# Performance work log

Hardware: AMD Instinct MI355X
Metric: run time of the kernel (lower is better)

Reference implementation:

```python
import jax, jax.numpy as jnp
import numpy as np

B, S, HID = 1, 2048, 4096
H, HKV, D = 32, 8, 128
ROT = 64  # partial_rotary_factor = 0.5
EPS = 1e-6
SCALE = D ** -0.5


def setup_inputs() -> dict:
    key = jax.random.key(0)
    ks = jax.random.split(key, 8)
    return {
        "hidden_states": jax.random.normal(ks[0], (B, S, HID), jnp.float32),
        "cos": jax.random.uniform(ks[1], (B, S, ROT), jnp.float32),
        "sin": jax.random.uniform(ks[2], (B, S, ROT), jnp.float32),
        "Wq": jax.random.normal(ks[3], (H * D, HID), jnp.float32) * 0.02,
        "Wk": jax.random.normal(ks[4], (HKV * D, HID), jnp.float32) * 0.02,
        "Wv": jax.random.normal(ks[5], (HKV * D, HID), jnp.float32) * 0.02,
        "Wo": jax.random.normal(ks[6], (H * D, HID), jnp.float32).T * 0.02,  # [HID, H*D]
        "q_norm_w": jnp.ones((D,), jnp.float32),
        "k_norm_w": jnp.ones((D,), jnp.float32),
    }


def _rmsnorm(x, w):
    var = jnp.mean(jnp.square(x), axis=-1, keepdims=True)
    return x * jax.lax.rsqrt(var + EPS) * w


def _rotate_half(x):
    x1, x2 = jnp.split(x, 2, axis=-1)
    return jnp.concatenate([-x2, x1], axis=-1)


def reference(hidden_states, cos, sin, Wq, Wk, Wv, Wo, q_norm_w, k_norm_w):
    b, s, _ = hidden_states.shape
    q = (hidden_states @ Wq.T).reshape(b, s, H, D)
    k = (hidden_states @ Wk.T).reshape(b, s, HKV, D)
    v = (hidden_states @ Wv.T).reshape(b, s, HKV, D)
    # per-head QK RMSNorm
    q = _rmsnorm(q, q_norm_w)
    k = _rmsnorm(k, k_norm_w)
    # partial RoPE on first ROT dims; cos/sin broadcast over head dim (unsqueeze_dim=2)
    cs = cos[:, :, None, :]  # [B,S,1,ROT]
    sn = sin[:, :, None, :]
    q_rot, q_pass = q[..., :ROT], q[..., ROT:]
    k_rot, k_pass = k[..., :ROT], k[..., ROT:]
    q_rot = q_rot * cs + _rotate_half(q_rot) * sn
    k_rot = k_rot * cs + _rotate_half(k_rot) * sn
    q = jnp.concatenate([q_rot, q_pass], axis=-1)
    k = jnp.concatenate([k_rot, k_pass], axis=-1)
    # GQA: expand kv heads to query heads
    rep = H // HKV
    k = jnp.repeat(k, rep, axis=2)  # [B,S,H,D]
    v = jnp.repeat(v, rep, axis=2)
    # causal SDPA, bsnd layout
    scores = jnp.einsum("bqhd,bkhd->bhqk", q, k) * SCALE
    causal = jnp.tril(jnp.ones((s, s), bool))
    scores = jnp.where(causal, scores, jnp.finfo(scores.dtype).min)
    attn = jax.nn.softmax(scores, axis=-1)
    out = jnp.einsum("bhqk,bkhd->bqhd", attn, v).reshape(b, s, H * D)
    return out @ Wo.T
```

## Files before the change

### kernel.cpp

```cpp
#include <hip/hip_runtime.h>
#include <hip/hip_bf16.h>

typedef __attribute__((ext_vector_type(8))) short bf16x8;
typedef __attribute__((ext_vector_type(4))) float f32x4;
typedef __hip_bfloat16 bf16;

#define S_LEN 2048
#define HIDDEN 4096
#define NH 32
#define NKV 8
#define DH 128
#define ROTD 64
#define QKVW 6144
#define KOFF 4096
#define VOFF 5120
#define ATT_SCALE 0.08838834764831845f
#define RMS_EPS 1e-6f
#define KPITCH 136
#define VPITCH 72

#define BAR() __builtin_amdgcn_s_barrier()
#define VMCNT(n) asm volatile("s_waitcnt vmcnt(" #n ")" ::: "memory")
#define LGKM(n)  asm volatile("s_waitcnt lgkmcnt(" #n ")" ::: "memory")

static __device__ __forceinline__ unsigned short f2bu(float f) {
    bf16 h = __float2bfloat16(f);
    return __builtin_bit_cast(unsigned short, h);
}

static __device__ __forceinline__ void load_lds_16(const bf16* g, bf16* l) {
    __builtin_amdgcn_global_load_lds((const __attribute__((address_space(1))) void*)g,
                                     (__attribute__((address_space(3))) void*)l, 16, 0, 0);
}

__global__ __launch_bounds__(256) void cast_f32_bf16(const float* __restrict__ src,
                                                     unsigned short* __restrict__ dst, int n4) {
    int i = blockIdx.x * 256 + threadIdx.x;
    if (i >= n4) return;
    float4 v = reinterpret_cast<const float4*>(src)[i];
    ushort4 o;
    o.x = f2bu(v.x); o.y = f2bu(v.y); o.z = f2bu(v.z); o.w = f2bu(v.w);
    reinterpret_cast<ushort4*>(dst)[i] = o;
}

__global__ __launch_bounds__(256) void add_f32(float* __restrict__ dst,
                                               const float* __restrict__ src, int n4) {
    int i = blockIdx.x * 256 + threadIdx.x;
    if (i >= n4) return;
    float4 a = reinterpret_cast<float4*>(dst)[i];
    float4 b = reinterpret_cast<const float4*>(src)[i];
    a.x += b.x; a.y += b.y; a.z += b.z; a.w += b.w;
    reinterpret_cast<float4*>(dst)[i] = a;
}

#define LDA_SUB(bufi, half) do {                                                        \
    const bf16* _ab = &As[bufi][half][0];                                               \
    _Pragma("unroll") for (int mf = 0; mf < 4; ++mf) {                                  \
        const int _r = arow + mf * 16;                                                  \
        _Pragma("unroll") for (int kk = 0; kk < 2; ++kk)                                \
            av[mf][kk] = *reinterpret_cast<const bf16x8*>(                              \
                _ab + (((_r << 6) + kk * 32 + quad * 8) ^ xorv));                       \
    } } while (0)

#define LDB_SUB(bufi, half, set) do {                                                   \
    const bf16* _bb = &Bs[bufi][half][0];                                               \
    _Pragma("unroll") for (int nf = 0; nf < 2; ++nf) {                                  \
        const int _r = brow + nf * 16;                                                  \
        _Pragma("unroll") for (int kk = 0; kk < 2; ++kk)                                \
            bv[set][nf][kk] = *reinterpret_cast<const bf16x8*>(                         \
                _bb + (((_r << 6) + kk * 32 + quad * 8) ^ xorv));                       \
    } } while (0)

#define MMQ(mh, nh, set) do {                                                           \
    _Pragma("unroll") for (int mf = 0; mf < 4; ++mf)                                    \
    _Pragma("unroll") for (int nf = 0; nf < 2; ++nf)                                    \
    _Pragma("unroll") for (int kk = 0; kk < 2; ++kk)                                    \
        acc[mh][nh][mf][nf] = __builtin_amdgcn_mfma_f32_16x16x32_bf16(                  \
            av[mf][kk], bv[set][nf][kk], acc[mh][nh][mf][nf], 0, 0, 0);                 \
    } while (0)

#define STAGE_A(bufi, half, tau) do {                                                   \
    const bf16* _s = Abase + (size_t)(half) * 128 * K + (size_t)(tau) * 64;             \
    load_lds_16(_s + sro0, &As[bufi][half][e0]);                                        \
    load_lds_16(_s + sro1, &As[bufi][half][e1]); } while (0)

#define STAGE_B(bufi, half, tau) do {                                                   \
    const bf16* _s = Bbase + (size_t)(half) * 128 * K + (size_t)(tau) * 64;             \
    load_lds_16(_s + sro0, &Bs[bufi][half][e0]);                                        \
    load_lds_16(_s + sro1, &Bs[bufi][half][e1]); } while (0)

template <typename OutT>
__global__ __launch_bounds__(512, 2) void gemm256(const bf16* __restrict__ A,
                                                  const bf16* __restrict__ B,
                                                  OutT* __restrict__ C,
                                                  OutT* __restrict__ C2,
                                                  int M, int N, int K, int ktiles) {
    __shared__ bf16 As[2][2][128 * 64];
    __shared__ bf16 Bs[2][2][128 * 64];

    const int tid  = threadIdx.x;
    const int lane = tid & 63;
    const int lq   = lane & 15;
    const int quad = lane >> 4;
    const int wave = tid >> 6;
    const int wr   = wave >> 2;
    const int wc   = wave & 3;

    const int nwg = gridDim.x;
    const int cpx = nwg >> 3;
    const int wg  = (blockIdx.x & 7) * cpx + (blockIdx.x >> 3);
    const int ntn = N >> 8;
    const int m0  = (wg / ntn) << 8;
    const int n0  = (wg % ntn) << 8;
    const int ksl = blockIdx.y;

    const int NT = ktiles;

    const int d0 = tid * 16;
    const int d1 = 8192 + tid * 16;
    const int o0 = d0 ^ (((d0 >> 7) & 7) << 4);
    const int o1 = d1 ^ (((d1 >> 7) & 7) << 4);
    const int e0 = d0 >> 1;
    const int e1 = d1 >> 1;
    const size_t sro0 = (size_t)((o0 >> 1) >> 6) * K + ((o0 >> 1) & 63);
    const size_t sro1 = (size_t)((o1 >> 1) >> 6) * K + ((o1 >> 1) & 63);
    const bf16* Abase = A + (size_t)m0 * K + (size_t)ksl * ktiles * 64;
    const bf16* Bbase = B + (size_t)n0 * K + (size_t)ksl * ktiles * 64;
    OutT* __restrict__ Cw = ksl ? C2 : C;

    const int arow = wr * 64 + lq;
    const int brow = wc * 32 + lq;
    const int xorv = (lq & 7) << 3;

    f32x4  acc[2][2][4][2] = {};
    bf16x8 av[4][2];
    bf16x8 bv[2][2][2];

    STAGE_B(0, 0, 0); STAGE_A(0, 0, 0); STAGE_B(0, 1, 0); STAGE_A(0, 1, 0);
    STAGE_B(1, 0, 1); STAGE_A(1, 0, 1); STAGE_B(1, 1, 1);
    VMCNT(6);
    BAR();

    for (int t = 0; t < NT; ++t) {
        const int buf = t & 1;

        LDA_SUB(buf, 0);
        LDB_SUB(buf, 0, 0);
        if (t + 1 < NT) STAGE_A(buf ^ 1, 1, t + 1);
        LGKM(8);
        BAR();
        LGKM(0);
        __builtin_amdgcn_s_setprio(1);
        MMQ(0, 0, 0);
        __builtin_amdgcn_s_setprio(0);
        BAR();

        LDB_SUB(buf, 1, 1);
        if (t + 2 < NT) STAGE_B(buf, 0, t + 2);
        BAR();
        LGKM(0);
        __builtin_amdgcn_s_setprio(1);
        MMQ(0, 1, 1);
        __builtin_amdgcn_s_setprio(0);
        BAR();

        LDA_SUB(buf, 1);
        if (t + 2 < NT) STAGE_A(buf, 0, t + 2);
        BAR();
        LGKM(0);
        __builtin_amdgcn_s_setprio(1);
        MMQ(1, 1, 1);
        __builtin_amdgcn_s_setprio(0);
        BAR();

        if (t + 2 < NT) STAGE_B(buf, 1, t + 2);
        BAR();
        __builtin_amdgcn_s_setprio(1);
        MMQ(1, 0, 0);
        __builtin_amdgcn_s_setprio(0);
        if (t < NT - 2) { VMCNT(6); } else { VMCNT(0); }
        BAR();
    }

#pragma unroll
    for (int mh = 0; mh < 2; ++mh)
#pragma unroll
        for (int nh = 0; nh < 2; ++nh)
#pragma unroll
            for (int mf = 0; mf < 4; ++mf)
#pragma unroll
                for (int nf = 0; nf < 2; ++nf)
#pragma unroll
                    for (int r = 0; r < 4; ++r) {
                        const int row = m0 + mh * 128 + wr * 64 + mf * 16 + quad * 4 + r;
                        const int col = n0 + nh * 128 + wc * 32 + nf * 16 + lq;
                        const float v = acc[mh][nh][mf][nf][r];
                        const size_t idx = (size_t)row * N + col;
                        if constexpr (sizeof(OutT) == 2) Cw[idx] = __float2bfloat16(v);
                        else                             Cw[idx] = v;
                    }
}

__global__ __launch_bounds__(256) void norm_rope(bf16* __restrict__ buf,
                                                 const float* __restrict__ w,
                                                 const float* __restrict__ cosp,
                                                 const float* __restrict__ sinp,
                                                 int log2nh, int stride, int coloff) {
    const int lane = threadIdx.x & 63;
    const int wave = threadIdx.x >> 6;
    const int row  = blockIdx.x * 4 + wave;
    const int s    = row >> log2nh;
    const int hh   = row & ((1 << log2nh) - 1);
    bf16* p = buf + (size_t)s * stride + coloff + hh * DH;

    float x1 = __bfloat162float(p[lane]);
    float x2 = __bfloat162float(p[64 + lane]);

    float ss = x1 * x1 + x2 * x2;
#pragma unroll
    for (int off = 1; off < 64; off <<= 1) ss += __shfl_xor(ss, off);
    float rs = rsqrtf(ss * (1.0f / 128.0f) + RMS_EPS);

    float y1 = x1 * rs * w[lane];
    float y2 = x2 * rs * w[64 + lane];

    float partner = __shfl_xor(y1, 32);
    float c  = cosp[(size_t)s * ROTD + lane];
    float sn = sinp[(size_t)s * ROTD + lane];
    float rot = (lane < 32) ? (y1 * c - partner * sn) : (y1 * c + partner * sn);

    p[lane]      = __float2bfloat16(rot);
    p[64 + lane] = __float2bfloat16(y2);
}

__global__ __launch_bounds__(256) void transpose_v(const bf16* __restrict__ v,
                                                   bf16* __restrict__ vt,
                                                   int stride, int colofs) {
    __shared__ bf16 t[32][65];
    const int c0 = blockIdx.x * 32;
    const int s0 = blockIdx.y * 64;
    {
        const int j  = threadIdx.x & 31;
        const int i0 = threadIdx.x >> 5;
#pragma unroll
        for (int p = 0; p < 8; ++p) {
            int si = p * 8 + i0;
            t[j][si] = v[(size_t)(s0 + si) * stride + colofs + c0 + j];
        }
    }
    __syncthreads();
    {
        const int ii = threadIdx.x & 63;
        const int j0 = threadIdx.x >> 6;
#pragma unroll
        for (int p = 0; p < 8; ++p) {
            int c = p * 4 + j0;
            vt[(size_t)(c0 + c) * S_LEN + s0 + ii] = t[c][ii];
        }
    }
}

struct FlashSmem {
    bf16 Ks[64][KPITCH];
    bf16 Vs[128][VPITCH];
    bf16 Ps[4][16][VPITCH];
};

static __device__ __forceinline__ void attn_qblock(int q0, int n_iter, int h, int kvh,
                                                   const bf16* __restrict__ QKV,
                                                   const bf16* __restrict__ VT,
                                                   bf16* __restrict__ O,
                                                   FlashSmem* sm) {
    const int tid  = threadIdx.x;
    const int lane = tid & 63;
    const int wave = tid >> 6;
    const int lq   = lane & 15;
    const int quad = lane >> 4;
    const int qr0  = q0 + wave * 16;

    bf16x8 qf[4];
    const bf16* qrow = QKV + (size_t)(qr0 + lq) * QKVW + h * DH + quad * 8;
#pragma unroll
    for (int i = 0; i < 4; ++i) {
        bf16x8 qv = *reinterpret_cast<const bf16x8*>(qrow + 32 * i);
#pragma unroll
        for (int j = 0; j < 8; ++j) {
            bf16 b = __builtin_bit_cast(bf16, (unsigned short)qv[j]);
            qv[j] = (short)__builtin_bit_cast(unsigned short,
                        __float2bfloat16(__bfloat162float(b) * ATT_SCALE));
        }
        qf[i] = qv;
    }

    f32x4 o[8];
#pragma unroll
    for (int t2 = 0; t2 < 8; ++t2) o[t2] = (f32x4){0.f, 0.f, 0.f, 0.f};
    float m_i[4], l_i[4];
#pragma unroll
    for (int r = 0; r < 4; ++r) { m_i[r] = -1e30f; l_i[r] = 0.f; }

    const bf16* kg = QKV + (size_t)(tid >> 2) * QKVW + KOFF + kvh * DH + (tid & 3) * 32;
    const bf16* vg = VT + (size_t)(kvh * DH + (tid >> 1)) * S_LEN + (tid & 1) * 32;
    bf16* ksl = &sm->Ks[tid >> 2][(tid & 3) * 32];
    bf16* vsl = &sm->Vs[tid >> 1][(tid & 1) * 32];
    bf16* pb  = &sm->Ps[wave][0][0];

    bf16x8 kreg[4], vreg[4];
#pragma unroll
    for (int c = 0; c < 4; ++c) {
        kreg[c] = *reinterpret_cast<const bf16x8*>(kg + 8 * c);
        vreg[c] = *reinterpret_cast<const bf16x8*>(vg + 8 * c);
    }

    for (int kt = 0; kt < n_iter; ++kt) {
        const int k0 = kt * 64;
#pragma unroll
        for (int c = 0; c < 4; ++c) {
            *reinterpret_cast<bf16x8*>(ksl + 8 * c) = kreg[c];
            *reinterpret_cast<bf16x8*>(vsl + 8 * c) = vreg[c];
        }
        __syncthreads();
        if (kt + 1 < n_iter) {
            const size_t kadv = (size_t)(kt + 1) * 64;
#pragma unroll
            for (int c = 0; c < 4; ++c) {
                kreg[c] = *reinterpret_cast<const bf16x8*>(kg + kadv * QKVW + 8 * c);
                vreg[c] = *reinterpret_cast<const bf16x8*>(vg + kadv + 8 * c);
            }
        }

        float p[4][4];
#pragma unroll
        for (int t = 0; t < 4; ++t) {
            f32x4 sacc = (f32x4){0.f, 0.f, 0.f, 0.f};
#pragma unroll
            for (int i = 0; i < 4; ++i) {
                bf16x8 kf = *reinterpret_cast<const bf16x8*>(&sm->Ks[t * 16 + lq][quad * 8 + 32 * i]);
                sacc = __builtin_amdgcn_mfma_f32_16x16x32_bf16(qf[i], kf, sacc, 0, 0, 0);
            }
#pragma unroll
            for (int r = 0; r < 4; ++r) {
                int qi = qr0 + quad * 4 + r;
                int ki = k0 + t * 16 + lq;
                p[t][r] = (ki > qi) ? -1e30f : sacc[r];
            }
        }

        float rowmax[4];
#pragma unroll
        for (int r = 0; r < 4; ++r)
            rowmax[r] = fmaxf(fmaxf(p[0][r], p[1][r]), fmaxf(p[2][r], p[3][r]));
#pragma unroll
        for (int off = 1; off < 16; off <<= 1)
#pragma unroll
            for (int r = 0; r < 4; ++r) rowmax[r] = fmaxf(rowmax[r], __shfl_xor(rowmax[r], off));

        float alpha[4];
#pragma unroll
        for (int r = 0; r < 4; ++r) {
            float mn = fmaxf(m_i[r], rowmax[r]);
            alpha[r] = __expf(m_i[r] - mn);
            m_i[r] = mn;
        }
#pragma unroll
        for (int t = 0; t < 4; ++t)
#pragma unroll
            for (int r = 0; r < 4; ++r) p[t][r] = __expf(p[t][r] - m_i[r]);

        float rsum[4];
#pragma unroll
        for (int r = 0; r < 4; ++r) rsum[r] = (p[0][r] + p[1][r]) + (p[2][r] + p[3][r]);
#pragma unroll
        for (int off = 1; off < 16; off <<= 1)
#pragma unroll
            for (int r = 0; r < 4; ++r) rsum[r] += __shfl_xor(rsum[r], off);
#pragma unroll
        for (int r = 0; r < 4; ++r) l_i[r] = l_i[r] * alpha[r] + rsum[r];

#pragma unroll
        for (int t = 0; t < 4; ++t)
#pragma unroll
            for (int r = 0; r < 4; ++r)
                pb[(quad * 4 + r) * VPITCH + t * 16 + lq] = __float2bfloat16(p[t][r]);
        __threadfence_block();

#pragma unroll
        for (int t2 = 0; t2 < 8; ++t2)
#pragma unroll
            for (int r = 0; r < 4; ++r) o[t2][r] *= alpha[r];

#pragma unroll
        for (int hh = 0; hh < 2; ++hh) {
            bf16x8 pa = *reinterpret_cast<const bf16x8*>(pb + lq * VPITCH + hh * 32 + quad * 8);
#pragma unroll
            for (int t2 = 0; t2 < 8; ++t2) {
                bf16x8 vf = *reinterpret_cast<const bf16x8*>(&sm->Vs[t2 * 16 + lq][hh * 32 + quad * 8]);
                o[t2] = __builtin_amdgcn_mfma_f32_16x16x32_bf16(pa, vf, o[t2], 0, 0, 0);
            }
        }
        __syncthreads();
    }

#pragma unroll
    for (int r = 0; r < 4; ++r) l_i[r] = 1.0f / l_i[r];
#pragma unroll
    for (int t2 = 0; t2 < 8; ++t2)
#pragma unroll
        for (int r = 0; r < 4; ++r)
            O[(size_t)(qr0 + quad * 4 + r) * (NH * DH) + h * DH + t2 * 16 + lq] =
                __float2bfloat16(o[t2][r] * l_i[r]);
}

__global__ __launch_bounds__(256) void flash_attn(const bf16* __restrict__ QKV,
                                                  const bf16* __restrict__ VT,
                                                  bf16* __restrict__ O) {
    __shared__ FlashSmem sm;
    const int b  = blockIdx.x;
    const int h  = b & 31;
    const int pr = b >> 5;
    const int kvh = h >> 2;
    attn_qblock((31 - pr) * 64, 32 - pr, h, kvh, QKV, VT, O, &sm);
    __syncthreads();
    attn_qblock(pr * 64,        pr + 1,  h, kvh, QKV, VT, O, &sm);
}

extern "C" void kernel_launch(void* const* d_in, const int* in_sizes, int n_in,
                              void* d_out, int out_size, void* d_ws, size_t ws_size,
                              hipStream_t stream) {
    const float* hs   = (const float*)d_in[0];
    const float* cosp = (const float*)d_in[1];
    const float* sinp = (const float*)d_in[2];
    const float* Wq   = (const float*)d_in[3];
    const float* Wk   = (const float*)d_in[4];
    const float* Wv   = (const float*)d_in[5];
    const float* Wo   = (const float*)d_in[6];
    const float* qw   = (const float*)d_in[7];
    const float* kw   = (const float*)d_in[8];
    float* out = (float*)d_out;

    char* ws = (char*)d_ws;
    size_t off = 0;
    auto carve = [&](size_t bytes) { char* p = ws + off; off += (bytes + 255) & ~(size_t)255; return p; };

    bf16* hsb  = (bf16*)carve((size_t)S_LEN * HIDDEN * 2);
    bf16* wqkv = (bf16*)carve((size_t)QKVW * HIDDEN * 2);
    bf16* wob  = (bf16*)carve((size_t)HIDDEN * NH * DH * 2);
    bf16* qkv  = (bf16*)carve((size_t)S_LEN * QKVW * 2);
    bf16* vtb  = (bf16*)carve((size_t)NKV * DH * S_LEN * 2);

    cast_f32_bf16<<<(S_LEN * HIDDEN / 4 + 255) / 256, 256, 0, stream>>>(hs, (unsigned short*)hsb, S_LEN * HIDDEN / 4);
    cast_f32_bf16<<<(NH * DH * HIDDEN / 4 + 255) / 256, 256, 0, stream>>>(Wq, (unsigned short*)wqkv, NH * DH * HIDDEN / 4);
    cast_f32_bf16<<<(NKV * DH * HIDDEN / 4 + 255) / 256, 256, 0, stream>>>(Wk, (unsigned short*)(wqkv + (size_t)KOFF * HIDDEN), NKV * DH * HIDDEN / 4);
    cast_f32_bf16<<<(NKV * DH * HIDDEN / 4 + 255) / 256, 256, 0, stream>>>(Wv, (unsigned short*)(wqkv + (size_t)VOFF * HIDDEN), NKV * DH * HIDDEN / 4);
    cast_f32_bf16<<<(HIDDEN * NH * DH / 4 + 255) / 256, 256, 0, stream>>>(Wo, (unsigned short*)wob, HIDDEN * NH * DH / 4);

    gemm256<bf16><<<dim3((S_LEN / 256) * (QKVW / 256), 1), 512, 0, stream>>>(
        hsb, wqkv, qkv, qkv, S_LEN, QKVW, HIDDEN, HIDDEN / 64);

    norm_rope<<<S_LEN * NH / 4, 256, 0, stream>>>(qkv, qw, cosp, sinp, 5, QKVW, 0);
    norm_rope<<<S_LEN * NKV / 4, 256, 0, stream>>>(qkv, kw, cosp, sinp, 3, QKVW, KOFF);

    transpose_v<<<dim3(NKV * DH / 32, S_LEN / 64), 256, 0, stream>>>(qkv, vtb, QKVW, VOFF);

    bf16* aob = hsb;
    flash_attn<<<512, 256, 0, stream>>>(qkv, vtb, aob);

    float* p1 = (float*)wqkv;
    gemm256<float><<<dim3((S_LEN / 256) * (HIDDEN / 256), 2), 512, 0, stream>>>(
        aob, wob, out, p1, S_LEN, HIDDEN, NH * DH, (NH * DH) / 2 / 64);

    add_f32<<<(S_LEN * HIDDEN / 4 + 255) / 256, 256, 0, stream>>>(out, p1, S_LEN * HIDDEN / 4);
}
```

Baseline: 539.7 us.

## Split attention KV range across two wave groups with LDS-direct swizzled K loads

The flash attention kernel now runs 512 threads per block, split into two groups of four waves that each process alternate 64-key tiles for the same query rows. Their partial softmax states are merged through LDS at the end. K tiles are loaded straight into LDS with XOR-swizzled global_load_lds, and V fragments are read directly from the transposed global buffer instead of being staged in LDS. This aims to raise parallelism and cut LDS staging cost. In exchange it adds a final merge step, exposes global-load latency on the V path, and idles one group on the last round when the tile count is odd.

New measurement: 607.7 us. 12.6% more time.

```diff
diff --git a/kernel.cpp b/kernel.cpp
--- a/kernel.cpp
+++ b/kernel.cpp
@@ -16,7 +16,6 @@
 #define VOFF 5120
 #define ATT_SCALE 0.08838834764831845f
 #define RMS_EPS 1e-6f
-#define KPITCH 136
 #define VPITCH 72
 
 #define BAR() __builtin_amdgcn_s_barrier()
@@ -261,9 +260,8 @@
 }
 
 struct FlashSmem {
-    bf16 Ks[64][KPITCH];
-    bf16 Vs[128][VPITCH];
-    bf16 Ps[4][16][VPITCH];
+    bf16 Ks[2][64][128];
+    bf16 Ps[8][16][VPITCH];
 };
 
 static __device__ __forceinline__ void attn_qblock(int q0, int n_iter, int h, int kvh,
@@ -274,9 +272,11 @@
     const int tid  = threadIdx.x;
     const int lane = tid & 63;
     const int wave = tid >> 6;
+    const int wq   = wave & 3;
+    const int g    = wave >> 2;
     const int lq   = lane & 15;
     const int quad = lane >> 4;
-    const int qr0  = q0 + wave * 16;
+    const int qr0  = q0 + wq * 16;
 
     bf16x8 qf[4];
     const bf16* qrow = QKV + (size_t)(qr0 + lq) * QKVW + h * DH + quad * 8;
@@ -285,9 +285,9 @@
         bf16x8 qv = *reinterpret_cast<const bf16x8*>(qrow + 32 * i);
 #pragma unroll
         for (int j = 0; j < 8; ++j) {
-            bf16 b = __builtin_bit_cast(bf16, (unsigned short)qv[j]);
+            bf16 bb = __builtin_bit_cast(bf16, (unsigned short)qv[j]);
             qv[j] = (short)__builtin_bit_cast(unsigned short,
-                        __float2bfloat16(__bfloat162float(b) * ATT_SCALE));
+                        __float2bfloat16(__bfloat162float(bb) * ATT_SCALE));
         }
         qf[i] = qv;
     }
@@ -299,121 +299,155 @@
 #pragma unroll
     for (int r = 0; r < 4; ++r) { m_i[r] = -1e30f; l_i[r] = 0.f; }
 
-    const bf16* kg = QKV + (size_t)(tid >> 2) * QKVW + KOFF + kvh * DH + (tid & 3) * 32;
-    const bf16* vg = VT + (size_t)(kvh * DH + (tid >> 1)) * S_LEN + (tid & 1) * 32;
-    bf16* ksl = &sm->Ks[tid >> 2][(tid & 3) * 32];
-    bf16* vsl = &sm->Vs[tid >> 1][(tid & 1) * 32];
+    const int d0 = tid * 16;
+    const int d1 = 8192 + tid * 16;
+    const int r0 = d0 >> 8;
+    const int r1 = d1 >> 8;
+    const int c0 = ((d0 ^ ((r0 & 7) << 4)) & 255) >> 1;
+    const int c1 = ((d1 ^ ((r1 & 7) << 4)) & 255) >> 1;
+    const bf16* Kg = QKV + (size_t)KOFF + kvh * DH;
+    const size_t so0 = (size_t)r0 * QKVW + c0;
+    const size_t so1 = (size_t)r1 * QKVW + c1;
+    bf16* ksb = &sm->Ks[0][0][0];
     bf16* pb  = &sm->Ps[wave][0][0];
-
-    bf16x8 kreg[4], vreg[4];
-#pragma unroll
-    for (int c = 0; c < 4; ++c) {
-        kreg[c] = *reinterpret_cast<const bf16x8*>(kg + 8 * c);
-        vreg[c] = *reinterpret_cast<const bf16x8*>(vg + 8 * c);
-    }
-
-    for (int kt = 0; kt < n_iter; ++kt) {
-        const int k0 = kt * 64;
-#pragma unroll
-        for (int c = 0; c < 4; ++c) {
-            *reinterpret_cast<bf16x8*>(ksl + 8 * c) = kreg[c];
-            *reinterpret_cast<bf16x8*>(vsl + 8 * c) = vreg[c];
-        }
-        __syncthreads();
-        if (kt + 1 < n_iter) {
-            const size_t kadv = (size_t)(kt + 1) * 64;
-#pragma unroll
-            for (int c = 0; c < 4; ++c) {
-                kreg[c] = *reinterpret_cast<const bf16x8*>(kg + kadv * QKVW + 8 * c);
-                vreg[c] = *reinterpret_cast<const bf16x8*>(vg + kadv + 8 * c);
+    const bf16* vb = VT + (size_t)(kvh * DH + lq) * S_LEN + quad * 8;
+
+    const int nrounds = (n_iter + 1) >> 1;
+    for (int rr = 0; rr < nrounds; ++rr) {
+        const int kt0 = 2 * rr;
+        {
+            const bf16* s0 = Kg + (size_t)kt0 * 64 * QKVW;
+            load_lds_16(s0 + so0, ksb + (d0 >> 1));
+            load_lds_16(s0 + so1, ksb + (d1 >> 1));
+            if (kt0 + 1 < n_iter) {
+                const bf16* s1 = s0 + (size_t)64 * QKVW;
+                load_lds_16(s1 + so0, ksb + 8192 + (d0 >> 1));
+                load_lds_16(s1 + so1, ksb + 8192 + (d1 >> 1));
             }
         }
-
-        float p[4][4];
-#pragma unroll
-        for (int t = 0; t < 4; ++t) {
-            f32x4 sacc = (f32x4){0.f, 0.f, 0.f, 0.f};
-#pragma unroll
-            for (int i = 0; i < 4; ++i) {
-                bf16x8 kf = *reinterpret_cast<const bf16x8*>(&sm->Ks[t * 16 + lq][quad * 8 + 32 * i]);
-                sacc = __builtin_amdgcn_mfma_f32_16x16x32_bf16(qf[i], kf, sacc, 0, 0, 0);
+        VMCNT(0);
+        BAR();
+
+        const int ktg = kt0 + g;
+        if (ktg < n_iter) {
+            const int k0 = ktg * 64;
+            const char* ksg = (const char*)(ksb + g * 8192);
+
+            float p[4][4];
+#pragma unroll
+            for (int t = 0; t < 4; ++t) {
+                f32x4 sacc = (f32x4){0.f, 0.f, 0.f, 0.f};
+#pragma unroll
+                for (int i = 0; i < 4; ++i) {
+                    const int krow = t * 16 + lq;
+                    const int kb = (krow << 8) + ((quad * 8 + 32 * i) << 1);
+                    bf16x8 kf = *reinterpret_cast<const bf16x8*>(ksg + (kb ^ ((krow & 7) << 4)));
+                    sacc = __builtin_amdgcn_mfma_f32_16x16x32_bf16(qf[i], kf, sacc, 0, 0, 0);
+                }
+#pragma unroll
+                for (int r = 0; r < 4; ++r) {
+                    int qi = qr0 + quad * 4 + r;
+                    int ki = k0 + t * 16 + lq;
+                    p[t][r] = (ki > qi) ? -1e30f : sacc[r];
+                }
             }
+
+            float rowmax[4];
+#pragma unroll
+            for (int r = 0; r < 4; ++r)
+                rowmax[r] = fmaxf(fmaxf(p[0][r], p[1][r]), fmaxf(p[2][r], p[3][r]));
+#pragma unroll
+            for (int off = 1; off < 16; off <<= 1)
+#pragma unroll
+                for (int r = 0; r < 4; ++r) rowmax[r] = fmaxf(rowmax[r], __shfl_xor(rowmax[r], off));
+
+            float alpha[4];
 #pragma unroll
             for (int r = 0; r < 4; ++r) {
-                int qi = qr0 + quad * 4 + r;
-                int ki = k0 + t * 16 + lq;
-                p[t][r] = (ki > qi) ? -1e30f : sacc[r];
+                float mn = fmaxf(m_i[r], rowmax[r]);
+                alpha[r] = __expf(m_i[r] - mn);
+                m_i[r] = mn;
             }
-        }
-
-        float rowmax[4];
-#pragma unroll
-        for (int r = 0; r < 4; ++r)
-            rowmax[r] = fmaxf(fmaxf(p[0][r], p[1][r]), fmaxf(p[2][r], p[3][r]));
-#pragma unroll
-        for (int off = 1; off < 16; off <<= 1)
-#pragma unroll
-            for (int r = 0; r < 4; ++r) rowmax[r] = fmaxf(rowmax[r], __shfl_xor(rowmax[r], off));
-
-        float alpha[4];
+#pragma unroll
+            for (int t = 0; t < 4; ++t)
+#pragma unroll
+                for (int r = 0; r < 4; ++r) p[t][r] = __expf(p[t][r] - m_i[r]);
+
+            float rsum[4];
+#pragma unroll
+            for (int r = 0; r < 4; ++r) rsum[r] = (p[0][r] + p[1][r]) + (p[2][r] + p[3][r]);
+#pragma unroll
+            for (int off = 1; off < 16; off <<= 1)
+#pragma unroll
+                for (int r = 0; r < 4; ++r) rsum[r] += __shfl_xor(rsum[r], off);
+#pragma unroll
+            for (int r = 0; r < 4; ++r) l_i[r] = l_i[r] * alpha[r] + rsum[r];
+
+#pragma unroll
+            for (int t = 0; t < 4; ++t)
+#pragma unroll
+                for (int r = 0; r < 4; ++r)
+                    pb[(quad * 4 + r) * VPITCH + t * 16 + lq] = __float2bfloat16(p[t][r]);
+            __threadfence_block();
+
+#pragma unroll
+            for (int t2 = 0; t2 < 8; ++t2)
+#pragma unroll
+                for (int r = 0; r < 4; ++r) o[t2][r] *= alpha[r];
+
+#pragma unroll
+            for (int hh = 0; hh < 2; ++hh) {
+                bf16x8 pa = *reinterpret_cast<const bf16x8*>(pb + lq * VPITCH + hh * 32 + quad * 8);
+#pragma unroll
+                for (int t2 = 0; t2 < 8; ++t2) {
+                    bf16x8 vf = *reinterpret_cast<const bf16x8*>(
+                        vb + (size_t)(t2 * 16) * S_LEN + k0 + hh * 32);
+                    o[t2] = __builtin_amdgcn_mfma_f32_16x16x32_bf16(pa, vf, o[t2], 0, 0, 0);
+                }
+            }
+        }
+        BAR();
+    }
+
+    float* osc = (float*)&sm->Ks[0][0][0];
+    float* mlc = (float*)&sm->Ps[0][0][0];
+    if (g == 1) {
+        const int wl = (wave - 4) * 64 + lane;
+#pragma unroll
+        for (int t2 = 0; t2 < 8; ++t2)
+            *reinterpret_cast<f32x4*>(osc + wl * 32 + t2 * 4) = o[t2];
+#pragma unroll
+        for (int r = 0; r < 4; ++r) { mlc[wl * 8 + r] = m_i[r]; mlc[wl * 8 + 4 + r] = l_i[r]; }
+    }
+    BAR();
+    if (g == 0) {
+        const int wl = wave * 64 + lane;
+        float sa[4], sb[4];
 #pragma unroll
         for (int r = 0; r < 4; ++r) {
-            float mn = fmaxf(m_i[r], rowmax[r]);
-            alpha[r] = __expf(m_i[r] - mn);
-            m_i[r] = mn;
-        }
-#pragma unroll
-        for (int t = 0; t < 4; ++t)
-#pragma unroll
-            for (int r = 0; r < 4; ++r) p[t][r] = __expf(p[t][r] - m_i[r]);
-
-        float rsum[4];
-#pragma unroll
-        for (int r = 0; r < 4; ++r) rsum[r] = (p[0][r] + p[1][r]) + (p[2][r] + p[3][r]);
-#pragma unroll
-        for (int off = 1; off < 16; off <<= 1)
-#pragma unroll
-            for (int r = 0; r < 4; ++r) rsum[r] += __shfl_xor(rsum[r], off);
-#pragma unroll
-        for (int r = 0; r < 4; ++r) l_i[r] = l_i[r] * alpha[r] + rsum[r];
-
-#pragma unroll
-        for (int t = 0; t < 4; ++t)
+            float mb = mlc[wl * 8 + r];
+            float lb = mlc[wl * 8 + 4 + r];
+            float mm = fmaxf(m_i[r], mb);
+            float ea = __expf(m_i[r] - mm);
+            float eb = __expf(mb - mm);
+            float inv = 1.0f / (l_i[r] * ea + lb * eb);
+            sa[r] = ea * inv;
+            sb[r] = eb * inv;
+        }
+#pragma unroll
+        for (int t2 = 0; t2 < 8; ++t2) {
+            f32x4 ob = *reinterpret_cast<const f32x4*>(osc + wl * 32 + t2 * 4);
 #pragma unroll
             for (int r = 0; r < 4; ++r)
-                pb[(quad * 4 + r) * VPITCH + t * 16 + lq] = __float2bfloat16(p[t][r]);
-        __threadfence_block();
-
-#pragma unroll
-        for (int t2 = 0; t2 < 8; ++t2)
-#pragma unroll
-            for (int r = 0; r < 4; ++r) o[t2][r] *= alpha[r];
-
-#pragma unroll
-        for (int hh = 0; hh < 2; ++hh) {
-            bf16x8 pa = *reinterpret_cast<const bf16x8*>(pb + lq * VPITCH + hh * 32 + quad * 8);
-#pragma unroll
-            for (int t2 = 0; t2 < 8; ++t2) {
-                bf16x8 vf = *reinterpret_cast<const bf16x8*>(&sm->Vs[t2 * 16 + lq][hh * 32 + quad * 8]);
-                o[t2] = __builtin_amdgcn_mfma_f32_16x16x32_bf16(pa, vf, o[t2], 0, 0, 0);
-            }
-        }
-        __syncthreads();
-    }
-
-#pragma unroll
-    for (int r = 0; r < 4; ++r) l_i[r] = 1.0f / l_i[r];
-#pragma unroll
-    for (int t2 = 0; t2 < 8; ++t2)
-#pragma unroll
-        for (int r = 0; r < 4; ++r)
-            O[(size_t)(qr0 + quad * 4 + r) * (NH * DH) + h * DH + t2 * 16 + lq] =
-                __float2bfloat16(o[t2][r] * l_i[r]);
-}
-
-__global__ __launch_bounds__(256) void flash_attn(const bf16* __restrict__ QKV,
-                                                  const bf16* __restrict__ VT,
-                                                  bf16* __restrict__ O) {
+                O[(size_t)(qr0 + quad * 4 + r) * (NH * DH) + h * DH + t2 * 16 + lq] =
+                    __float2bfloat16(o[t2][r] * sa[r] + ob[r] * sb[r]);
+        }
+    }
+}
+
+__global__ __launch_bounds__(512, 4) void flash_attn(const bf16* __restrict__ QKV,
+                                                     const bf16* __restrict__ VT,
+                                                     bf16* __restrict__ O) {
     __shared__ FlashSmem sm;
     const int b  = blockIdx.x;
     const int h  = b & 31;
@@ -463,7 +497,7 @@
     transpose_v<<<dim3(NKV * DH / 32, S_LEN / 64), 256, 0, stream>>>(qkv, vtb, QKVW, VOFF);
 
     bf16* aob = hsb;
-    flash_attn<<<512, 256, 0, stream>>>(qkv, vtb, aob);
+    flash_attn<<<512, 512, 0, stream>>>(qkv, vtb, aob);
 
     float* p1 = (float*)wqkv;
     gemm256<float><<<dim3((S_LEN / 256) * (HIDDEN / 256), 2), 512, 0, stream>>>(
```
